# Kernel tuning notes

Hardware: AMD Instinct MI355X
Metric: run time of the kernel (lower is better)

The kernel has to match this reference:

```python
import jax, jax.numpy as jnp
import numpy as np

N_EMBED = 384
NUM_EXPERTS = 8
TOP_K = 2


def setup_inputs() -> dict:
    key = jax.random.key(0)
    k_x, k_n, k_w1, k_b1, k_w2, k_b2 = jax.random.split(key, 6)
    B, T = 16, 4096
    bound = 1.0 / np.sqrt(N_EMBED)
    return {
        "x": jax.random.normal(k_x, (B, T, N_EMBED), dtype=jnp.float32),
        "noise": jax.random.normal(k_n, (B, T, NUM_EXPERTS), dtype=jnp.float32),
        "w_route": jax.random.uniform(k_w1, (NUM_EXPERTS, N_EMBED), jnp.float32, -bound, bound),
        "b_route": jax.random.uniform(k_b1, (NUM_EXPERTS,), jnp.float32, -bound, bound),
        "w_noise": jax.random.uniform(k_w2, (NUM_EXPERTS, N_EMBED), jnp.float32, -bound, bound),
        "b_noise": jax.random.uniform(k_b2, (NUM_EXPERTS,), jnp.float32, -bound, bound),
    }


def reference(x, noise, w_route, b_route, w_noise, b_noise):
    # two tiny linears: [B,T,D] @ [D,E] -> [B,T,E]
    logits = jnp.einsum("btd,ed->bte", x, w_route) + b_route
    noise_logits = jnp.einsum("btd,ed->bte", x, w_noise) + b_noise
    noisy_logits = logits + noise * jax.nn.softplus(noise_logits)

    top_k_logits, indices = jax.lax.top_k(noisy_logits, TOP_K)  # [B,T,k]

    # scatter top-k values into a -inf tensor; equivalently mask non-topk to -inf
    # (values at the top-k positions are exactly the noisy logits there)
    mask = jax.nn.one_hot(indices, NUM_EXPERTS, dtype=jnp.bool_).any(axis=-2)  # [B,T,E]
    sparse_logits = jnp.where(mask, noisy_logits, -jnp.inf)
    router_output = jax.nn.softmax(sparse_logits, axis=-1)
    return router_output, indices
```

## Files before the change

kernel.cpp:

```cpp
#include <hip/hip_runtime.h>
#include <math.h>


constexpr int D = 384;

__global__ __launch_bounds__(256) void noisy_topk_router_f32(
    const float* __restrict__ x,
    const float* __restrict__ noise,
    const float* __restrict__ w_route,
    const float* __restrict__ b_route,
    const float* __restrict__ w_noise,
    const float* __restrict__ b_noise,
    float* __restrict__ out,
    int ntok)
{
    __shared__ float w_lds[16 * D];
    __shared__ float bias[16];

    const int tid = threadIdx.x;

#pragma unroll
    for (int r = 0; r < 3; ++r) {
        int i = (tid + 256 * r) * 4;
        *(float4*)(w_lds + i)            = *(const float4*)(w_route + i);
        *(float4*)(w_lds + 3072 + i)     = *(const float4*)(w_noise + i);
    }
    if (tid < 8)       bias[tid] = b_route[tid];
    else if (tid < 16) bias[tid] = b_noise[tid - 8];
    __syncthreads();

    const int wave = tid >> 6;
    const int lane = tid & 63;
    const int tg   = lane >> 3;
    const int c    = lane & 7;
    const int tok0 = blockIdx.x * 128 + wave * 32 + tg * 4;

    float acc[4][16];
#pragma unroll
    for (int t = 0; t < 4; ++t)
#pragma unroll
        for (int e = 0; e < 16; ++e) acc[t][e] = 0.f;

    const float* xbase = x + (size_t)tok0 * D + c * 4;
#pragma unroll 2
    for (int j = 0; j < 12; ++j) {
        const int dbase = j * 32;
        float4 xv0 = *(const float4*)(xbase + dbase);
        float4 xv1 = *(const float4*)(xbase + D + dbase);
        float4 xv2 = *(const float4*)(xbase + 2 * D + dbase);
        float4 xv3 = *(const float4*)(xbase + 3 * D + dbase);
#pragma unroll
        for (int e = 0; e < 16; ++e) {
            float4 wv = *(const float4*)(w_lds + e * D + dbase + c * 4);
            acc[0][e] += xv0.x * wv.x + xv0.y * wv.y + xv0.z * wv.z + xv0.w * wv.w;
            acc[1][e] += xv1.x * wv.x + xv1.y * wv.y + xv1.z * wv.z + xv1.w * wv.w;
            acc[2][e] += xv2.x * wv.x + xv2.y * wv.y + xv2.z * wv.z + xv2.w * wv.w;
            acc[3][e] += xv3.x * wv.x + xv3.y * wv.y + xv3.z * wv.z + xv3.w * wv.w;
        }
    }

#pragma unroll
    for (int t = 0; t < 4; ++t)
#pragma unroll
        for (int e = 0; e < 16; ++e) {
            acc[t][e] += __shfl_xor(acc[t][e], 1);
            acc[t][e] += __shfl_xor(acc[t][e], 2);
            acc[t][e] += __shfl_xor(acc[t][e], 4);
        }

    if (c < 4) {
        const int token = tok0 + c;
        float4 n0 = *(const float4*)(noise + (size_t)token * 8);
        float4 n1 = *(const float4*)(noise + (size_t)token * 8 + 4);
        float nz[8] = {n0.x, n0.y, n0.z, n0.w, n1.x, n1.y, n1.z, n1.w};

        float noisy[8];
#pragma unroll
        for (int e = 0; e < 8; ++e) {
            float lg = acc[c][e] + bias[e];
            float nl = acc[c][8 + e] + bias[8 + e];
            float sp = fmaxf(nl, 0.f) + log1pf(expf(-fabsf(nl)));
            noisy[e] = lg + nz[e] * sp;
        }

        float v0 = noisy[0]; int i0 = 0;
#pragma unroll
        for (int e = 1; e < 8; ++e)
            if (noisy[e] > v0) { v0 = noisy[e]; i0 = e; }
        float v1 = -INFINITY; int i1 = 0;
#pragma unroll
        for (int e = 0; e < 8; ++e)
            if (e != i0 && noisy[e] > v1) { v1 = noisy[e]; i1 = e; }

        float ex  = expf(v1 - v0);
        float inv = 1.f / (1.f + ex);
        float p0  = inv;
        float p1  = ex * inv;

        float pr[8];
#pragma unroll
        for (int e = 0; e < 8; ++e)
            pr[e] = (e == i0) ? p0 : ((e == i1) ? p1 : 0.f);

        float* orow = out + (size_t)token * 8;
        *(float4*)(orow)     = make_float4(pr[0], pr[1], pr[2], pr[3]);
        *(float4*)(orow + 4) = make_float4(pr[4], pr[5], pr[6], pr[7]);

        *(float2*)(out + (size_t)ntok * 8 + (size_t)token * 2) =
            make_float2((float)i0, (float)i1);
    }
}

extern "C" void kernel_launch(void* const* d_in, const int* in_sizes, int n_in,
                              void* d_out, int out_size, void* d_ws, size_t ws_size,
                              hipStream_t stream) {
    const float* x       = (const float*)d_in[0];
    const float* noise   = (const float*)d_in[1];
    const float* w_route = (const float*)d_in[2];
    const float* b_route = (const float*)d_in[3];
    const float* w_noise = (const float*)d_in[4];
    const float* b_noise = (const float*)d_in[5];
    float* out = (float*)d_out;

    const int ntok   = in_sizes[0] / D;
    const int blocks = ntok / 128;

    hipLaunchKernelGGL(noisy_topk_router_f32, dim3(blocks), dim3(256), 0, stream,
                       x, noise, w_route, b_route, w_noise, b_noise, out, ntok);
}
```

Before: 181.7 us.

## Widen lane split per token, prefetch x, and use DPP transpose-reduce

Each group of four tokens is now handled by 16 lanes instead of 8, halving tokens per block and doubling the grid. The x loads are double-buffered in registers across the reduction loop. The cross-lane reduction is reworked into a transposing DPP/ds_swizzle scheme that sums four token partials with fewer exchange instructions. An occupancy hint is added to launch bounds; the kernel is likely already near memory bandwidth limits, so gains are uncertain.

```diff
diff --git a/kernel.cpp b/kernel.cpp
--- a/kernel.cpp
+++ b/kernel.cpp
@@ -4,7 +4,22 @@
 
 constexpr int D = 384;
 
-__global__ __launch_bounds__(256) void noisy_topk_router_f32(
+__device__ __forceinline__ float dpp_xor1(float v) {
+    return __int_as_float(__builtin_amdgcn_update_dpp(
+        0, __float_as_int(v), 0xB1, 0xF, 0xF, true));
+}
+__device__ __forceinline__ float dpp_xor2(float v) {
+    return __int_as_float(__builtin_amdgcn_update_dpp(
+        0, __float_as_int(v), 0x4E, 0xF, 0xF, true));
+}
+__device__ __forceinline__ float swz_xor4(float v) {
+    return __int_as_float(__builtin_amdgcn_ds_swizzle(__float_as_int(v), 0x101F));
+}
+__device__ __forceinline__ float swz_xor8(float v) {
+    return __int_as_float(__builtin_amdgcn_ds_swizzle(__float_as_int(v), 0x201F));
+}
+
+__global__ __launch_bounds__(256, 4) void noisy_topk_router_f32(
     const float* __restrict__ x,
     const float* __restrict__ noise,
     const float* __restrict__ w_route,
@@ -22,8 +37,8 @@
 #pragma unroll
     for (int r = 0; r < 3; ++r) {
         int i = (tid + 256 * r) * 4;
-        *(float4*)(w_lds + i)            = *(const float4*)(w_route + i);
-        *(float4*)(w_lds + 3072 + i)     = *(const float4*)(w_noise + i);
+        *(float4*)(w_lds + i)        = *(const float4*)(w_route + i);
+        *(float4*)(w_lds + 3072 + i) = *(const float4*)(w_noise + i);
     }
     if (tid < 8)       bias[tid] = b_route[tid];
     else if (tid < 16) bias[tid] = b_noise[tid - 8];
@@ -31,9 +46,9 @@
 
     const int wave = tid >> 6;
     const int lane = tid & 63;
-    const int tg   = lane >> 3;
-    const int c    = lane & 7;
-    const int tok0 = blockIdx.x * 128 + wave * 32 + tg * 4;
+    const int tg   = lane >> 4;
+    const int c    = lane & 15;
+    const int tok0 = blockIdx.x * 64 + wave * 16 + tg * 4;
 
     float acc[4][16];
 #pragma unroll
@@ -41,32 +56,52 @@
 #pragma unroll
         for (int e = 0; e < 16; ++e) acc[t][e] = 0.f;
 
-    const float* xbase = x + (size_t)tok0 * D + c * 4;
-#pragma unroll 2
-    for (int j = 0; j < 12; ++j) {
-        const int dbase = j * 32;
-        float4 xv0 = *(const float4*)(xbase + dbase);
-        float4 xv1 = *(const float4*)(xbase + D + dbase);
-        float4 xv2 = *(const float4*)(xbase + 2 * D + dbase);
-        float4 xv3 = *(const float4*)(xbase + 3 * D + dbase);
+    const float* xr = x + (size_t)tok0 * D + c * 4;
+
+    float4 xv[4], xn[4];
+#pragma unroll
+    for (int t = 0; t < 4; ++t) xv[t] = *(const float4*)(xr + t * D);
+
+#pragma unroll 1
+    for (int j = 0; j < 6; ++j) {
+        const int jn = (j < 5) ? (j + 1) * 64 : 0;
+#pragma unroll
+        for (int t = 0; t < 4; ++t) xn[t] = *(const float4*)(xr + t * D + jn);
+
+        const float* wj = w_lds + j * 64 + c * 4;
 #pragma unroll
         for (int e = 0; e < 16; ++e) {
-            float4 wv = *(const float4*)(w_lds + e * D + dbase + c * 4);
-            acc[0][e] += xv0.x * wv.x + xv0.y * wv.y + xv0.z * wv.z + xv0.w * wv.w;
-            acc[1][e] += xv1.x * wv.x + xv1.y * wv.y + xv1.z * wv.z + xv1.w * wv.w;
-            acc[2][e] += xv2.x * wv.x + xv2.y * wv.y + xv2.z * wv.z + xv2.w * wv.w;
-            acc[3][e] += xv3.x * wv.x + xv3.y * wv.y + xv3.z * wv.z + xv3.w * wv.w;
+            float4 wv = *(const float4*)(wj + e * D);
+            acc[0][e] += xv[0].x * wv.x + xv[0].y * wv.y + xv[0].z * wv.z + xv[0].w * wv.w;
+            acc[1][e] += xv[1].x * wv.x + xv[1].y * wv.y + xv[1].z * wv.z + xv[1].w * wv.w;
+            acc[2][e] += xv[2].x * wv.x + xv[2].y * wv.y + xv[2].z * wv.z + xv[2].w * wv.w;
+            acc[3][e] += xv[3].x * wv.x + xv[3].y * wv.y + xv[3].z * wv.z + xv[3].w * wv.w;
         }
+#pragma unroll
+        for (int t = 0; t < 4; ++t) xv[t] = xn[t];
     }
 
+    const bool b0 = (c & 1), b1 = (c >> 1) & 1;
+    float a2[2][16];
 #pragma unroll
-    for (int t = 0; t < 4; ++t)
+    for (int u = 0; u < 2; ++u)
 #pragma unroll
         for (int e = 0; e < 16; ++e) {
-            acc[t][e] += __shfl_xor(acc[t][e], 1);
-            acc[t][e] += __shfl_xor(acc[t][e], 2);
-            acc[t][e] += __shfl_xor(acc[t][e], 4);
+            float s = b0 ? acc[2 * u][e]     : acc[2 * u + 1][e];
+            float k = b0 ? acc[2 * u + 1][e] : acc[2 * u][e];
+            a2[u][e] = k + dpp_xor1(s);
         }
+    float a1[16];
+#pragma unroll
+    for (int e = 0; e < 16; ++e) {
+        float s = b1 ? a2[0][e] : a2[1][e];
+        float k = b1 ? a2[1][e] : a2[0][e];
+        a1[e] = k + dpp_xor2(s);
+    }
+#pragma unroll
+    for (int e = 0; e < 16; ++e) a1[e] += swz_xor4(a1[e]);
+#pragma unroll
+    for (int e = 0; e < 16; ++e) a1[e] += swz_xor8(a1[e]);
 
     if (c < 4) {
         const int token = tok0 + c;
@@ -77,8 +112,8 @@
         float noisy[8];
 #pragma unroll
         for (int e = 0; e < 8; ++e) {
-            float lg = acc[c][e] + bias[e];
-            float nl = acc[c][8 + e] + bias[8 + e];
+            float lg = a1[e] + bias[e];
+            float nl = a1[8 + e] + bias[8 + e];
             float sp = fmaxf(nl, 0.f) + log1pf(expf(-fabsf(nl)));
             noisy[e] = lg + nz[e] * sp;
         }
@@ -123,7 +158,7 @@
     float* out = (float*)d_out;
 
     const int ntok   = in_sizes[0] / D;
-    const int blocks = ntok / 128;
+    const int blocks = ntok / 64;
 
     hipLaunchKernelGGL(noisy_topk_router_f32, dim3(blocks), dim3(256), 0, stream,
                        x, noise, w_route, b_route, w_noise, b_noise, out, ntok);
```

New measurement: 214.2 us. +17.9%, slower.
